# Optimization experiments

Hardware: AMD Instinct MI355X
Metric: run time of the kernel (lower is better)

The kernel has to match this reference:

```python
import jax, jax.numpy as jnp
import numpy as np

N_ATOM_TYPES = 100
N_BOND_TYPES = 10
N_NODES = 10000
N_EDGES = 320000
N_CAND = 100000
HID = 256
N_MP = 3


def setup_inputs() -> dict:
    key = jax.random.key(0)
    ks = jax.random.split(key, 16)
    d = HID
    inp = {
        "atom_types": jax.random.randint(ks[0], (N_NODES,), 0, N_ATOM_TYPES),
        "bond_types": jax.random.randint(ks[1], (N_EDGES,), 0, N_BOND_TYPES),
        "edge_index": jax.random.randint(ks[2], (2, N_EDGES), 0, N_NODES),
        "candidates": jax.random.randint(ks[3], (N_CAND, 2), 0, N_NODES),
        # parameters (weights stored as [in, out]; bias [out])
        "atom_embed": jax.random.normal(ks[4], (N_ATOM_TYPES, d)) * 0.02,
        "atom_W": jax.random.normal(ks[5], (d, d)) / np.sqrt(d),
        "atom_b": jnp.zeros((d,)),
        "bond_embed": jax.random.normal(ks[6], (N_BOND_TYPES, d)) * 0.02,
        "bond_W": jax.random.normal(ks[7], (d, d)) / np.sqrt(d),
        "bond_b": jnp.zeros((d,)),
        "conv_W": jax.random.normal(ks[8], (N_MP, d, d)) / np.sqrt(d),
        "conv_b": jnp.zeros((N_MP, d)),
        "s_W1": jax.random.normal(ks[9], (2 * d, d)) / np.sqrt(2 * d),
        "s_b1": jnp.zeros((d,)),
        "s_W2": jax.random.normal(ks[10], (d, 1)) / np.sqrt(d),
        "s_b2": jnp.zeros((1,)),
    }
    return inp


def _wln_forward(atom_types, bond_types, edge_index, candidates,
                 atom_embed, atom_W, atom_b, bond_embed, bond_W, bond_b,
                 conv_W, conv_b, s_W1, s_b1, s_W2, s_b2):
    # encoders
    h = atom_embed[atom_types] @ atom_W + atom_b            # [N, d]
    e = bond_embed[bond_types] @ bond_W + bond_b            # [E, d] (unused downstream, as in the original forward)
    del e

    src, dst = edge_index[0], edge_index[1]
    n = h.shape[0]
    ones = jnp.ones((src.shape[0],), dtype=h.dtype)
    deg_out = jax.ops.segment_sum(ones, src, num_segments=n)
    deg_in = jax.ops.segment_sum(ones, dst, num_segments=n)
    norm_src = jnp.where(deg_out > 0, deg_out ** -0.5, 0.0)[:, None]  # [N,1]
    norm_dst = jnp.where(deg_in > 0, deg_in ** -0.5, 0.0)[:, None]

    # message passing: DGL GraphConv norm='both' + ReLU
    for i in range(conv_W.shape[0]):
        m = (h * norm_src)[src]                             # [E, d]
        agg = jax.ops.segment_sum(m, dst, num_segments=n)   # [N, d]
        h = jax.nn.relu((agg * norm_dst) @ conv_W[i] + conv_b[i])

    # batched candidate scorer: gather + concat + 2-layer MLP
    u, v = candidates[:, 0], candidates[:, 1]
    pair = jnp.concatenate([h[u], h[v]], axis=-1)           # [C, 2d]
    hid = jax.nn.relu(pair @ s_W1 + s_b1)                   # [C, d]
    scores = hid @ s_W2 + s_b2                              # [C, 1]
    return scores.squeeze(-1)                               # [C]


def reference(atom_types, bond_types, edge_index, candidates,
              atom_embed, atom_W, atom_b, bond_embed, bond_W, bond_b,
              conv_W, conv_b, s_W1, s_b1, s_W2, s_b2):
    return _wln_forward(atom_types, bond_types, edge_index, candidates,
                        atom_embed, atom_W, atom_b, bond_embed, bond_W, bond_b,
                        conv_W, conv_b, s_W1, s_b1, s_W2, s_b2)
```

## Files before the change

### kernel.cpp

```cpp
#include <hip/hip_runtime.h>

#define N_NODES 10000
#define N_EDGES 320000
#define N_CAND  100000
#define HID     256
#define N_MP    3
#define N_ATYPE 100

static __device__ __forceinline__ float relu_f(float x) { return x > 0.f ? x : 0.f; }

static __device__ __forceinline__ void gemm_core(
    const float* __restrict__ A, const float* __restrict__ B,
    const float* __restrict__ bias, const float* __restrict__ scale,
    float* __restrict__ C, int M, int mb, int nb, int doRelu)
{
    __shared__ float As[32][68];
    __shared__ float Bs[32][68];

    int tid = threadIdx.x;
    int tx = tid & 15;
    int ty = tid >> 4;

    float acc[8][4] = {};

    for (int k0 = 0; k0 < 256; k0 += 32) {
        #pragma unroll
        for (int p = 0; p < 4; ++p) {
            int flat = p * 128 + tid;
            int row  = flat >> 3;
            int kc   = flat & 7;
            float4 av = make_float4(0.f, 0.f, 0.f, 0.f);
            if (mb + row < M)
                av = *(const float4*)(A + (size_t)(mb + row) * 256 + k0 + kc * 4);
            As[kc * 4 + 0][row] = av.x;
            As[kc * 4 + 1][row] = av.y;
            As[kc * 4 + 2][row] = av.z;
            As[kc * 4 + 3][row] = av.w;
        }
        #pragma unroll
        for (int p = 0; p < 4; ++p) {
            int flat = p * 128 + tid;
            int row  = flat >> 4;
            int c    = flat & 15;
            *(float4*)(&Bs[row][c * 4]) =
                *(const float4*)(B + (size_t)(k0 + row) * 256 + nb + c * 4);
        }
        __syncthreads();

        #pragma unroll
        for (int k = 0; k < 32; ++k) {
            float4 a0 = *(const float4*)(&As[k][ty * 8]);
            float4 a1 = *(const float4*)(&As[k][ty * 8 + 4]);
            float4 b4 = *(const float4*)(&Bs[k][tx * 4]);
            float a[8] = {a0.x, a0.y, a0.z, a0.w, a1.x, a1.y, a1.z, a1.w};
            float b[4] = {b4.x, b4.y, b4.z, b4.w};
            #pragma unroll
            for (int i = 0; i < 8; ++i)
                #pragma unroll
                for (int j = 0; j < 4; ++j)
                    acc[i][j] = fmaf(a[i], b[j], acc[i][j]);
        }
        __syncthreads();
    }

    float bvv[4] = {0.f, 0.f, 0.f, 0.f};
    if (bias) {
        float4 bv = *(const float4*)(bias + nb + tx * 4);
        bvv[0] = bv.x; bvv[1] = bv.y; bvv[2] = bv.z; bvv[3] = bv.w;
    }
    #pragma unroll
    for (int i = 0; i < 8; ++i) {
        int row = mb + ty * 8 + i;
        if (row >= M) continue;
        float sc = scale ? scale[row] : 1.0f;
        float r[4];
        #pragma unroll
        for (int j = 0; j < 4; ++j) {
            r[j] = acc[i][j] + bvv[j];
            if (doRelu) r[j] = relu_f(r[j]);
            r[j] *= sc;
        }
        *(float4*)(C + (size_t)row * 256 + nb + tx * 4) =
            make_float4(r[0], r[1], r[2], r[3]);
    }
}

__global__ __launch_bounds__(128) void k_gemm(
    const float* __restrict__ A, const float* __restrict__ B,
    const float* __restrict__ bias, float* __restrict__ C,
    int M, int doRelu)
{
    gemm_core(A, B, bias, nullptr, C, M, blockIdx.x * 64, blockIdx.y * 64, doRelu);
}

__global__ __launch_bounds__(128) void k_gemm_conv(
    const float* __restrict__ A, const float* __restrict__ B,
    const float* __restrict__ bias, const float* __restrict__ scale,
    float* __restrict__ C, int M)
{
    int bid = blockIdx.x;
    int l = bid & 7;
    int r = bid >> 3;
    int y = r & 3;
    int g = r >> 2;
    int x = g * 8 + l;
    if (x * 64 >= M) return;
    gemm_core(A, B, bias, scale, C, M, x * 64, y * 64, 1);
}

__global__ __launch_bounds__(128) void k_gemm_pq(
    const float* __restrict__ A, const float* __restrict__ W1,
    float* __restrict__ P, float* __restrict__ Q, int M)
{
    int bid = blockIdx.x;
    int l = bid & 7;
    int r = bid >> 3;
    int y = r & 7;
    int g = r >> 3;
    int x = g * 8 + l;
    if (x * 64 >= M) return;
    int half = y >> 2;
    const float* B = W1 + (size_t)half * 256 * 256;
    float* C = half ? Q : P;
    gemm_core(A, B, nullptr, nullptr, C, M, x * 64, (y & 3) * 64, 0);
}

__global__ void k_hist(const int* __restrict__ ei,
                       int* __restrict__ dout, int* __restrict__ din)
{
    int e = blockIdx.x * blockDim.x + threadIdx.x;
    if (e >= N_EDGES) return;
    atomicAdd(&dout[ei[e]], 1);
    atomicAdd(&din[ei[N_EDGES + e]], 1);
}

__global__ void k_norm(const int* __restrict__ dout, const int* __restrict__ din,
                       float* __restrict__ ns, float* __restrict__ nd)
{
    int i = blockIdx.x * blockDim.x + threadIdx.x;
    if (i >= N_NODES) return;
    int o = dout[i], in = din[i];
    ns[i] = (o  > 0) ? (1.0f / sqrtf((float)o))  : 0.f;
    nd[i] = (in > 0) ? (1.0f / sqrtf((float)in)) : 0.f;
}

__global__ __launch_bounds__(256) void k_h0(const int* __restrict__ types,
                                            const float* __restrict__ E0,
                                            const float* __restrict__ ns,
                                            float* __restrict__ h)
{
    int node = blockIdx.x * 4 + (threadIdx.x >> 6);
    int lane = threadIdx.x & 63;
    if (node >= N_NODES) return;
    int t = types[node];
    float s = ns[node];
    float4 v = ((const float4*)E0)[t * 64 + lane];
    v.x *= s; v.y *= s; v.z *= s; v.w *= s;
    ((float4*)h)[node * 64 + lane] = v;
}

__global__ __launch_bounds__(1024) void k_scan(const int* __restrict__ deg,
                                               int* __restrict__ off, int n)
{
    __shared__ int part[1024];
    int t = threadIdx.x;
    int chunk = (n + 1023) / 1024;
    int base = t * chunk;
    int s = 0;
    for (int i = 0; i < chunk; ++i) {
        int idx = base + i;
        if (idx < n) s += deg[idx];
    }
    part[t] = s;
    __syncthreads();
    for (int d = 1; d < 1024; d <<= 1) {
        int v = (t >= d) ? part[t - d] : 0;
        __syncthreads();
        part[t] += v;
        __syncthreads();
    }
    int run = (t == 0) ? 0 : part[t - 1];
    if (t == 0) off[0] = 0;
    for (int i = 0; i < chunk; ++i) {
        int idx = base + i;
        if (idx < n) { run += deg[idx]; off[idx + 1] = run; }
    }
}

__global__ void k_fill(const int* __restrict__ ei, const int* __restrict__ off,
                       int* __restrict__ cur, int* __restrict__ csr)
{
    int e = blockIdx.x * blockDim.x + threadIdx.x;
    if (e >= N_EDGES) return;
    int d = ei[N_EDGES + e];
    int p = off[d] + atomicAdd(&cur[d], 1);
    csr[p] = ei[e];
}

__global__ __launch_bounds__(256) void k_agg(
    const float* __restrict__ h, const float* __restrict__ nd,
    const int* __restrict__ off, const int* __restrict__ csr,
    float* __restrict__ out)
{
    int bid  = blockIdx.x;
    int slot = bid & 7;
    int c    = slot >> 1;
    int grp  = ((bid >> 3) << 1) | (slot & 1);
    int wave = threadIdx.x >> 6;
    int lane = threadIdx.x & 63;
    int node = grp * 4 + wave;
    int col  = c * 64 + lane;

    int s0 = off[node], s1 = off[node + 1];
    float acc0 = 0.f, acc1 = 0.f, acc2 = 0.f, acc3 = 0.f;
    int e = s0;
    for (; e + 4 <= s1; e += 4) {
        int i0 = csr[e], i1 = csr[e + 1], i2 = csr[e + 2], i3 = csr[e + 3];
        float v0 = h[(size_t)i0 * 256 + col];
        float v1 = h[(size_t)i1 * 256 + col];
        float v2 = h[(size_t)i2 * 256 + col];
        float v3 = h[(size_t)i3 * 256 + col];
        acc0 += v0; acc1 += v1; acc2 += v2; acc3 += v3;
    }
    for (; e < s1; ++e)
        acc0 += h[(size_t)csr[e] * 256 + col];
    out[(size_t)node * 256 + col] = (acc0 + acc1 + acc2 + acc3) * nd[node];
}

__global__ __launch_bounds__(256) void k_score_part(
    const int* __restrict__ cand, const float* __restrict__ P,
    const float* __restrict__ Q, const float* __restrict__ b1,
    const float* __restrict__ W2, float* __restrict__ part)
{
    int bid  = blockIdx.x;
    int c    = bid & 7;
    int grp  = bid >> 3;
    int wave = threadIdx.x >> 6;
    int lane = threadIdx.x & 63;
    int half = lane >> 5;
    int l    = lane & 31;
    int cd   = grp * 8 + wave * 2 + half;
    int col  = c * 32 + l;

    int u = cand[2 * cd];
    int v = cand[2 * cd + 1];
    float x = P[(size_t)u * 256 + col] + Q[(size_t)v * 256 + col] + b1[col];
    x = relu_f(x) * W2[col];
    #pragma unroll
    for (int o = 16; o > 0; o >>= 1)
        x += __shfl_xor(x, o, 64);
    if (l == 0) part[(size_t)c * N_CAND + cd] = x;
}

__global__ void k_sred(const float* __restrict__ part,
                       const float* __restrict__ b2, float* __restrict__ out)
{
    int i = blockIdx.x * 256 + threadIdx.x;
    if (i >= N_CAND) return;
    float s = b2[0];
    #pragma unroll
    for (int c = 0; c < 8; ++c) s += part[(size_t)c * N_CAND + i];
    out[i] = s;
}

extern "C" void kernel_launch(void* const* d_in, const int* in_sizes, int n_in,
                              void* d_out, int out_size, void* d_ws, size_t ws_size,
                              hipStream_t stream)
{
    const int*   atom_types = (const int*)d_in[0];
    const int*   edge_index = (const int*)d_in[2];
    const int*   candidates = (const int*)d_in[3];
    const float* atom_embed = (const float*)d_in[4];
    const float* atom_W     = (const float*)d_in[5];
    const float* atom_b     = (const float*)d_in[6];
    const float* conv_W     = (const float*)d_in[10];
    const float* conv_b     = (const float*)d_in[11];
    const float* s_W1       = (const float*)d_in[12];
    const float* s_b1       = (const float*)d_in[13];
    const float* s_W2       = (const float*)d_in[14];
    const float* s_b2       = (const float*)d_in[15];
    float* out = (float*)d_out;

    char* w = (char*)d_ws;
    size_t o = 0;
    auto alloc = [&](size_t bytes) {
        void* p = w + o;
        o += (bytes + 255) & ~(size_t)255;
        return p;
    };
    float* h0   = (float*)alloc((size_t)N_NODES * HID * 4);
    float* h1   = (float*)alloc((size_t)N_NODES * HID * 4);
    float* agg  = (float*)alloc((size_t)N_NODES * HID * 4);
    float* E0   = (float*)alloc((size_t)N_ATYPE * HID * 4);
    float* part = (float*)alloc((size_t)8 * N_CAND * 4);
    int*   ints = (int*)alloc((size_t)3 * N_NODES * 4);
    float* ns   = (float*)alloc((size_t)N_NODES * 4);
    float* nd   = (float*)alloc((size_t)N_NODES * 4);
    int*   off  = (int*)alloc((size_t)(N_NODES + 1) * 4);
    int*   csr  = (int*)alloc((size_t)N_EDGES * 4);
    int* dego = ints;
    int* degi = ints + N_NODES;
    int* cur  = ints + 2 * N_NODES;

    hipMemsetAsync(ints, 0, (size_t)3 * N_NODES * 4, stream);

    k_gemm<<<dim3(2, 4), 128, 0, stream>>>(atom_embed, atom_W, atom_b, E0, N_ATYPE, 0);

    k_hist<<<(N_EDGES + 255) / 256, 256, 0, stream>>>(edge_index, dego, degi);
    k_norm<<<(N_NODES + 255) / 256, 256, 0, stream>>>(dego, degi, ns, nd);
    k_h0<<<N_NODES / 4, 256, 0, stream>>>(atom_types, E0, ns, h0);
    k_scan<<<1, 1024, 0, stream>>>(degi, off, N_NODES);
    k_fill<<<(N_EDGES + 255) / 256, 256, 0, stream>>>(edge_index, off, cur, csr);

    const float* hc = h0;
    float* hn = h1;
    for (int i = 0; i < N_MP; ++i) {
        k_agg<<<N_NODES, 256, 0, stream>>>(hc, nd, off, csr, agg);
        const float* sc = (i < N_MP - 1) ? ns : nullptr;
        k_gemm_conv<<<640, 128, 0, stream>>>(
            agg, conv_W + (size_t)i * HID * HID, conv_b + (size_t)i * HID,
            sc, hn, N_NODES);
        float* t = (float*)hc; hc = hn; hn = t;
    }
    float* P = agg;
    float* Q = hn;
    k_gemm_pq<<<1280, 128, 0, stream>>>(hc, s_W1, P, Q, N_NODES);

    k_score_part<<<N_CAND, 256, 0, stream>>>(candidates, P, Q, s_b1, s_W2, part);
    k_sred<<<(N_CAND + 255) / 256, 256, 0, stream>>>(part, s_b2, out);
}
```

Baseline: 418.2 us.

## Split-K conv GEMM with 256-thread tiles and per-thread candidate scoring

The GEMM core moves to 256 threads with a 4x4 per-thread tile and a 64-wide K step. The conv GEMM is split into two K halves written to separate buffers, and a new elementwise kernel adds them with bias, ReLU and scaling. The candidate scorer now has each thread handle one candidate over a 32-column chunk with float4 loads, instead of a wave-shuffle reduction. This aims to raise occupancy and parallelism, but adds an extra pass over a full N×256 buffer and halves per-thread arithmetic reuse in the GEMM.

Measured after the change: 372.1 us. 1.12x faster.

```diff
diff --git a/kernel.cpp b/kernel.cpp
--- a/kernel.cpp
+++ b/kernel.cpp
@@ -12,23 +12,24 @@
 static __device__ __forceinline__ void gemm_core(
     const float* __restrict__ A, const float* __restrict__ B,
     const float* __restrict__ bias, const float* __restrict__ scale,
-    float* __restrict__ C, int M, int mb, int nb, int doRelu)
-{
-    __shared__ float As[32][68];
-    __shared__ float Bs[32][68];
+    float* __restrict__ C, int M, int mb, int nb,
+    int kbase, int klen, int doRelu)
+{
+    __shared__ float As[64][68];
+    __shared__ float Bs[64][64];
 
     int tid = threadIdx.x;
     int tx = tid & 15;
     int ty = tid >> 4;
 
-    float acc[8][4] = {};
-
-    for (int k0 = 0; k0 < 256; k0 += 32) {
+    float acc[4][4] = {};
+
+    for (int k0 = kbase; k0 < kbase + klen; k0 += 64) {
         #pragma unroll
         for (int p = 0; p < 4; ++p) {
-            int flat = p * 128 + tid;
-            int row  = flat >> 3;
-            int kc   = flat & 7;
+            int flat = p * 256 + tid;
+            int row  = flat >> 4;
+            int kc   = flat & 15;
             float4 av = make_float4(0.f, 0.f, 0.f, 0.f);
             if (mb + row < M)
                 av = *(const float4*)(A + (size_t)(mb + row) * 256 + k0 + kc * 4);
@@ -39,7 +40,7 @@
         }
         #pragma unroll
         for (int p = 0; p < 4; ++p) {
-            int flat = p * 128 + tid;
+            int flat = p * 256 + tid;
             int row  = flat >> 4;
             int c    = flat & 15;
             *(float4*)(&Bs[row][c * 4]) =
@@ -47,15 +48,14 @@
         }
         __syncthreads();
 
-        #pragma unroll
-        for (int k = 0; k < 32; ++k) {
-            float4 a0 = *(const float4*)(&As[k][ty * 8]);
-            float4 a1 = *(const float4*)(&As[k][ty * 8 + 4]);
+        #pragma unroll 16
+        for (int k = 0; k < 64; ++k) {
+            float4 a4 = *(const float4*)(&As[k][ty * 4]);
             float4 b4 = *(const float4*)(&Bs[k][tx * 4]);
-            float a[8] = {a0.x, a0.y, a0.z, a0.w, a1.x, a1.y, a1.z, a1.w};
+            float a[4] = {a4.x, a4.y, a4.z, a4.w};
             float b[4] = {b4.x, b4.y, b4.z, b4.w};
             #pragma unroll
-            for (int i = 0; i < 8; ++i)
+            for (int i = 0; i < 4; ++i)
                 #pragma unroll
                 for (int j = 0; j < 4; ++j)
                     acc[i][j] = fmaf(a[i], b[j], acc[i][j]);
@@ -69,8 +69,8 @@
         bvv[0] = bv.x; bvv[1] = bv.y; bvv[2] = bv.z; bvv[3] = bv.w;
     }
     #pragma unroll
-    for (int i = 0; i < 8; ++i) {
-        int row = mb + ty * 8 + i;
+    for (int i = 0; i < 4; ++i) {
+        int row = mb + ty * 4 + i;
         if (row >= M) continue;
         float sc = scale ? scale[row] : 1.0f;
         float r[4];
@@ -85,30 +85,52 @@
     }
 }
 
-__global__ __launch_bounds__(128) void k_gemm(
+__global__ __launch_bounds__(256) void k_gemm(
     const float* __restrict__ A, const float* __restrict__ B,
     const float* __restrict__ bias, float* __restrict__ C,
     int M, int doRelu)
 {
-    gemm_core(A, B, bias, nullptr, C, M, blockIdx.x * 64, blockIdx.y * 64, doRelu);
-}
-
-__global__ __launch_bounds__(128) void k_gemm_conv(
+    gemm_core(A, B, bias, nullptr, C, M, blockIdx.x * 64, blockIdx.y * 64,
+              0, 256, doRelu);
+}
+
+__global__ __launch_bounds__(256) void k_gemm_conv(
     const float* __restrict__ A, const float* __restrict__ B,
-    const float* __restrict__ bias, const float* __restrict__ scale,
-    float* __restrict__ C, int M)
+    float* __restrict__ C0, float* __restrict__ C1, int M)
 {
     int bid = blockIdx.x;
     int l = bid & 7;
     int r = bid >> 3;
-    int y = r & 3;
-    int g = r >> 2;
-    int x = g * 8 + l;
+    int ks = r & 1;
+    int y  = (r >> 1) & 3;
+    int g  = r >> 3;
+    int x  = g * 8 + l;
     if (x * 64 >= M) return;
-    gemm_core(A, B, bias, scale, C, M, x * 64, y * 64, 1);
-}
-
-__global__ __launch_bounds__(128) void k_gemm_pq(
+    float* C = ks ? C1 : C0;
+    gemm_core(A, B, nullptr, nullptr, C, M, x * 64, y * 64, ks * 128, 128, 0);
+}
+
+__global__ __launch_bounds__(256) void k_combine(
+    float* __restrict__ C0, const float* __restrict__ C1,
+    const float* __restrict__ bias, const float* __restrict__ scale)
+{
+    int i = blockIdx.x * 256 + threadIdx.x;
+    if (i >= N_NODES * 64) return;
+    int row  = i >> 6;
+    int col4 = i & 63;
+    float4 a = ((const float4*)C0)[i];
+    float4 b = ((const float4*)C1)[i];
+    float4 bv = ((const float4*)bias)[col4];
+    float sc = scale ? scale[row] : 1.0f;
+    float4 r;
+    r.x = relu_f(a.x + b.x + bv.x) * sc;
+    r.y = relu_f(a.y + b.y + bv.y) * sc;
+    r.z = relu_f(a.z + b.z + bv.z) * sc;
+    r.w = relu_f(a.w + b.w + bv.w) * sc;
+    ((float4*)C0)[i] = r;
+}
+
+__global__ __launch_bounds__(256) void k_gemm_pq(
     const float* __restrict__ A, const float* __restrict__ W1,
     float* __restrict__ P, float* __restrict__ Q, int M)
 {
@@ -122,7 +144,7 @@
     int half = y >> 2;
     const float* B = W1 + (size_t)half * 256 * 256;
     float* C = half ? Q : P;
-    gemm_core(A, B, nullptr, nullptr, C, M, x * 64, (y & 3) * 64, 0);
+    gemm_core(A, B, nullptr, nullptr, C, M, x * 64, (y & 3) * 64, 0, 256, 0);
 }
 
 __global__ void k_hist(const int* __restrict__ ei,
@@ -232,24 +254,34 @@
     const float* __restrict__ Q, const float* __restrict__ b1,
     const float* __restrict__ W2, float* __restrict__ part)
 {
-    int bid  = blockIdx.x;
-    int c    = bid & 7;
-    int grp  = bid >> 3;
-    int wave = threadIdx.x >> 6;
-    int lane = threadIdx.x & 63;
-    int half = lane >> 5;
-    int l    = lane & 31;
-    int cd   = grp * 8 + wave * 2 + half;
-    int col  = c * 32 + l;
+    int bid = blockIdx.x;
+    int c   = bid & 7;
+    int grp = bid >> 3;
+    int cd  = grp * 256 + threadIdx.x;
+    if (cd >= N_CAND) return;
 
     int u = cand[2 * cd];
     int v = cand[2 * cd + 1];
-    float x = P[(size_t)u * 256 + col] + Q[(size_t)v * 256 + col] + b1[col];
-    x = relu_f(x) * W2[col];
+    const float4* P4 = (const float4*)P;
+    const float4* Q4 = (const float4*)Q;
+    const float4* B4 = (const float4*)b1;
+    const float4* W4 = (const float4*)W2;
+    size_t pb = (size_t)u * 64 + c * 8;
+    size_t qb = (size_t)v * 64 + c * 8;
+
+    float acc = 0.f;
     #pragma unroll
-    for (int o = 16; o > 0; o >>= 1)
-        x += __shfl_xor(x, o, 64);
-    if (l == 0) part[(size_t)c * N_CAND + cd] = x;
+    for (int i = 0; i < 8; ++i) {
+        float4 p = P4[pb + i];
+        float4 q = Q4[qb + i];
+        float4 b = B4[c * 8 + i];
+        float4 w = W4[c * 8 + i];
+        acc = fmaf(relu_f(p.x + q.x + b.x), w.x, acc);
+        acc = fmaf(relu_f(p.y + q.y + b.y), w.y, acc);
+        acc = fmaf(relu_f(p.z + q.z + b.z), w.z, acc);
+        acc = fmaf(relu_f(p.w + q.w + b.w), w.w, acc);
+    }
+    part[(size_t)c * N_CAND + cd] = acc;
 }
 
 __global__ void k_sred(const float* __restrict__ part,
@@ -291,6 +323,7 @@
     float* h0   = (float*)alloc((size_t)N_NODES * HID * 4);
     float* h1   = (float*)alloc((size_t)N_NODES * HID * 4);
     float* agg  = (float*)alloc((size_t)N_NODES * HID * 4);
+    float* ctmp = (float*)alloc((size_t)N_NODES * HID * 4);
     float* E0   = (float*)alloc((size_t)N_ATYPE * HID * 4);
     float* part = (float*)alloc((size_t)8 * N_CAND * 4);
     int*   ints = (int*)alloc((size_t)3 * N_NODES * 4);
@@ -304,7 +337,7 @@
 
     hipMemsetAsync(ints, 0, (size_t)3 * N_NODES * 4, stream);
 
-    k_gemm<<<dim3(2, 4), 128, 0, stream>>>(atom_embed, atom_W, atom_b, E0, N_ATYPE, 0);
+    k_gemm<<<dim3(2, 4), 256, 0, stream>>>(atom_embed, atom_W, atom_b, E0, N_ATYPE, 0);
 
     k_hist<<<(N_EDGES + 255) / 256, 256, 0, stream>>>(edge_index, dego, degi);
     k_norm<<<(N_NODES + 255) / 256, 256, 0, stream>>>(dego, degi, ns, nd);
@@ -314,18 +347,20 @@
 
     const float* hc = h0;
     float* hn = h1;
+    const int NF4 = N_NODES * 64;
     for (int i = 0; i < N_MP; ++i) {
         k_agg<<<N_NODES, 256, 0, stream>>>(hc, nd, off, csr, agg);
+        k_gemm_conv<<<1280, 256, 0, stream>>>(
+            agg, conv_W + (size_t)i * HID * HID, hn, ctmp, N_NODES);
         const float* sc = (i < N_MP - 1) ? ns : nullptr;
-        k_gemm_conv<<<640, 128, 0, stream>>>(
-            agg, conv_W + (size_t)i * HID * HID, conv_b + (size_t)i * HID,
-            sc, hn, N_NODES);
+        k_combine<<<(NF4 + 255) / 256, 256, 0, stream>>>(
+            hn, ctmp, conv_b + (size_t)i * HID, sc);
         float* t = (float*)hc; hc = hn; hn = t;
     }
     float* P = agg;
     float* Q = hn;
-    k_gemm_pq<<<1280, 128, 0, stream>>>(hc, s_W1, P, Q, N_NODES);
-
-    k_score_part<<<N_CAND, 256, 0, stream>>>(candidates, P, Q, s_b1, s_W2, part);
+    k_gemm_pq<<<1280, 256, 0, stream>>>(hc, s_W1, P, Q, N_NODES);
+
+    k_score_part<<<3128, 256, 0, stream>>>(candidates, P, Q, s_b1, s_W2, part);
     k_sred<<<(N_CAND + 255) / 256, 256, 0, stream>>>(part, s_b2, out);
 }
```
